# Kernel tuning notes

Measured on AMD Instinct MI355X. Metric: run time of the kernel, lower is better.

Reference implementation:

```python
import jax, jax.numpy as jnp
import numpy as np

T, B, H, L = 512, 64, 100, 10  # seq_len, batch, hidden, num_layers


def setup_inputs() -> dict:
    key = jax.random.key(0)
    ks = jax.random.split(key, 8)
    s = 0.1  # ~ PyTorch uniform(-1/sqrt(H), 1/sqrt(H)) scale
    return {
        "x": jax.random.normal(ks[0], (T, B, H), jnp.float32),
        "W_ih0": jax.random.normal(ks[1], (2, H, H), jnp.float32) * s,
        "W_ih": jax.random.normal(ks[2], (L - 1, 2, H, 2 * H), jnp.float32) * s,
        "W_hh": jax.random.normal(ks[3], (L, 2, H, H), jnp.float32) * s,
        "b_ih": jax.random.normal(ks[4], (L, 2, H), jnp.float32) * s,
        "b_hh": jax.random.normal(ks[5], (L, 2, H), jnp.float32) * s,
        "W_out": jax.random.normal(ks[6], (1, 2 * H), jnp.float32) * s,
        "b_out": jax.random.normal(ks[7], (1,), jnp.float32) * s,
    }


def _rnn_dir(x, Wih, Whh, b, reverse):
    # Precompute input projection for all timesteps as one big GEMM.
    # z: [T, B, H]; b already holds b_ih + b_hh.
    z = jnp.einsum('tbi,hi->tbh', x, Wih) + b
    h0 = jnp.zeros((x.shape[1], Whh.shape[0]), x.dtype)

    def step(h, zt):
        h = jnp.tanh(zt + h @ Whh.T)
        return h, h

    # reverse=True scans backward in time but emits outputs in original order,
    # exactly matching the backward direction of a bidirectional RNN.
    _, ys = jax.lax.scan(step, h0, z, reverse=reverse)
    return ys  # [T, B, H]


def reference(x, W_ih0, W_ih, W_hh, b_ih, b_hh, W_out, b_out):
    h = x
    for l in range(L):
        Wih_l = W_ih0 if l == 0 else W_ih[l - 1]
        fwd = _rnn_dir(h, Wih_l[0], W_hh[l, 0], b_ih[l, 0] + b_hh[l, 0], False)
        bwd = _rnn_dir(h, Wih_l[1], W_hh[l, 1], b_ih[l, 1] + b_hh[l, 1], True)
        h = jnp.concatenate([fwd, bwd], axis=-1)  # [T, B, 2H]
    y = jax.nn.sigmoid(jnp.einsum('tbh,oh->tbo', h, W_out) + b_out)  # [T, B, 1]
    return y.reshape(-1)  # [T*B]
```

## Files before the change

### kernel.cpp

```cpp
#include <hip/hip_runtime.h>
#include <math.h>


#define T_LEN 512
#define BATCH 64
#define HID   100
#define M_TOT (T_LEN * BATCH)

__global__ __launch_bounds__(256) void ingemm_kernel(
    const float* __restrict__ In, const float* __restrict__ W,
    const float* __restrict__ bih, const float* __restrict__ bhh,
    float* __restrict__ z, int K)
{
    __shared__ float As[16][68];
    __shared__ float Bs[16][68];
    const int tid = threadIdx.x;
    const int m0 = blockIdx.x * 64;
    const int n0 = blockIdx.y * 64;
    const int tx = tid & 15, ty = tid >> 4;
    const int lm = tid >> 2;
    const int lk = (tid & 3) << 2;

    float acc[4][4];
    #pragma unroll
    for (int i = 0; i < 4; ++i)
        #pragma unroll
        for (int j = 0; j < 4; ++j) acc[i][j] = 0.f;

    for (int k0 = 0; k0 < K; k0 += 16) {
        float4 av = make_float4(0.f,0.f,0.f,0.f);
        float4 bv = make_float4(0.f,0.f,0.f,0.f);
        if (k0 + lk < K)
            av = *(const float4*)(In + (size_t)(m0 + lm) * K + k0 + lk);
        const int nrow = n0 + lm;
        if (nrow < 200 && k0 + lk < K)
            bv = *(const float4*)(W + (size_t)nrow * K + k0 + lk);
        As[lk+0][lm]=av.x; As[lk+1][lm]=av.y; As[lk+2][lm]=av.z; As[lk+3][lm]=av.w;
        Bs[lk+0][lm]=bv.x; Bs[lk+1][lm]=bv.y; Bs[lk+2][lm]=bv.z; Bs[lk+3][lm]=bv.w;
        __syncthreads();
        #pragma unroll
        for (int kk = 0; kk < 16; ++kk) {
            float4 a4 = *(const float4*)&As[kk][ty << 2];
            float4 b4 = *(const float4*)&Bs[kk][tx << 2];
            float a[4] = {a4.x, a4.y, a4.z, a4.w};
            float b[4] = {b4.x, b4.y, b4.z, b4.w};
            #pragma unroll
            for (int i = 0; i < 4; ++i)
                #pragma unroll
                for (int j = 0; j < 4; ++j)
                    acc[i][j] += a[i] * b[j];
        }
        __syncthreads();
    }
    #pragma unroll
    for (int i = 0; i < 4; ++i) {
        const int m = m0 + (ty << 2) + i;
        #pragma unroll
        for (int j = 0; j < 4; ++j) {
            const int n = n0 + (tx << 2) + j;
            if (n < 200) {
                const int dir = (n >= 100) ? 1 : 0;
                const int h = n - dir * 100;
                z[(size_t)dir * M_TOT * HID + (size_t)m * HID + h] =
                    acc[i][j] + bih[n] + bhh[n];
            }
        }
    }
}

__device__ __forceinline__ float dpp_qxor1(float x) {
    int i = __float_as_int(x);
    i = __builtin_amdgcn_update_dpp(0, i, 0xB1, 0xF, 0xF, false);
    return __int_as_float(i);
}
__device__ __forceinline__ float dpp_qxor2(float x) {
    int i = __float_as_int(x);
    i = __builtin_amdgcn_update_dpp(0, i, 0x4E, 0xF, 0xF, false);
    return __int_as_float(i);
}

__global__ __launch_bounds__(256) void scan_kernel(
    const float* __restrict__ z,
    const float* __restrict__ Whh,
    float* __restrict__ out)
{
    const int dir = blockIdx.x >> 6;
    const int b   = blockIdx.x & 63;
    const int tid = threadIdx.x;
    const int w   = tid >> 6;
    const int lane= tid & 63;
    const int ks  = lane & 3;
    const int jslot = lane >> 2;
    const int jj  = w + 4 * jslot;
    const bool active = (jj < 50);
    const int jjc = active ? jj : 49;
    const int kb  = 28 * ks;
    const int jout = 2 * jjc + (ks & 1);
    const bool writer = active && (ks < 2);

    __shared__ float h_lds[2][128];
    for (int i = tid; i < 256; i += 256) (&h_lds[0][0])[i] = 0.f;

    float w2[2][28];
    #pragma unroll
    for (int r = 0; r < 2; ++r) {
        const float* wr = Whh + ((size_t)dir * HID + 2 * jjc + r) * HID + kb;
        #pragma unroll
        for (int q = 0; q < 7; ++q) {
            float4 v = make_float4(0.f, 0.f, 0.f, 0.f);
            if (kb + 4 * q + 3 < HID)
                v = *(const float4*)(wr + 4 * q);
            w2[r][4*q+0] = v.x; w2[r][4*q+1] = v.y;
            w2[r][4*q+2] = v.z; w2[r][4*q+3] = v.w;
        }
    }
    __syncthreads();

    const ptrdiff_t zstride = BATCH * HID;
    const ptrdiff_t ostride = BATCH * 200;
    const int t0 = dir ? (T_LEN - 1) : 0;
    const ptrdiff_t zstep = dir ? -zstride : zstride;
    const ptrdiff_t ostep = dir ? -ostride : ostride;
    const ptrdiff_t zstep2 = 2 * zstep, zstep3 = 3 * zstep, zstep4 = 4 * zstep;

    const float* zp = z + (size_t)dir * M_TOT * HID + (size_t)b * HID + jout
                        + (ptrdiff_t)t0 * zstride;
    float*       op = out + (size_t)b * 200 + dir * HID + jout
                        + (ptrdiff_t)t0 * ostride;

    float zr0 = zp[0];
    float zr1 = zp[zstep];
    float zr2 = zp[zstep2];
    float zr3 = zp[zstep3];
    const float* zpf = zp + zstep4;

#define RNN_STEP(ZREG, DO_PF, PFOFF, RD, WRB)                           \
  do {                                                                  \
    const float zin = ZREG;                                             \
    if (DO_PF) ZREG = *(zpf + (PFOFF));   \
    const float4* hp = (const float4*)((RD) + kb);                      \
    float a0 = 0.f, a1 = 0.f;                                           \
    _Pragma("unroll")                                                   \
    for (int q = 0; q < 7; ++q) {                                       \
      float4 hv = hp[q];                                                \
      a0 += w2[0][4*q+0] * hv.x; a0 += w2[0][4*q+1] * hv.y;             \
      a0 += w2[0][4*q+2] * hv.z; a0 += w2[0][4*q+3] * hv.w;             \
      a1 += w2[1][4*q+0] * hv.x; a1 += w2[1][4*q+1] * hv.y;             \
      a1 += w2[1][4*q+2] * hv.z; a1 += w2[1][4*q+3] * hv.w;             \
    }                                                                   \
            \
    float keep = (ks & 1) ? a1 : a0;                                    \
    float send = (ks & 1) ? a0 : a1;                                    \
    float s = keep + dpp_qxor1(send);                                   \
          \
    float tot = s + dpp_qxor2(s);                                       \
    float xin = zin + tot;                                              \
    float ax = fabsf(xin);                                              \
    float e = __expf(2.f * ax);                                         \
    float r = 1.f - 2.f / (e + 1.f);                                    \
    float val = copysignf(r, xin);                                      \
    if (writer) {                                                       \
      (WRB)[jout] = val;                                                \
      *op = val;                                                        \
    }                                                                   \
    op += ostep;                                                        \
    asm volatile("s_waitcnt lgkmcnt(0)" ::: "memory");                  \
    __builtin_amdgcn_sched_barrier(0);                                  \
    __builtin_amdgcn_s_barrier();                                       \
    __builtin_amdgcn_sched_barrier(0);                                  \
  } while (0)

    float* const h0 = &h_lds[0][0];
    float* const h1 = &h_lds[1][0];

    for (int g = 0; g < (T_LEN / 4) - 1; ++g) {
        RNN_STEP(zr0, 1, 0,      h0, h1);
        RNN_STEP(zr1, 1, zstep,  h1, h0);
        RNN_STEP(zr2, 1, zstep2, h0, h1);
        RNN_STEP(zr3, 1, zstep3, h1, h0);
        zpf += zstep4;
    }
    RNN_STEP(zr0, 0, 0, h0, h1);
    RNN_STEP(zr1, 0, 0, h1, h0);
    RNN_STEP(zr2, 0, 0, h0, h1);
    RNN_STEP(zr3, 0, 0, h1, h0);

#undef RNN_STEP
}

__global__ __launch_bounds__(256) void outproj_kernel(
    const float* __restrict__ h, const float* __restrict__ Wout,
    const float* __restrict__ bout, float* __restrict__ y)
{
    const int gid = blockIdx.x * 256 + threadIdx.x;
    const int wid = gid >> 6;
    const int lane = threadIdx.x & 63;
    if (wid >= M_TOT) return;
    const float* row = h + (size_t)wid * 200;
    float acc = 0.f;
    for (int k = lane; k < 200; k += 64) acc += row[k] * Wout[k];
    #pragma unroll
    for (int off = 32; off > 0; off >>= 1) acc += __shfl_xor(acc, off);
    if (lane == 0) y[wid] = 1.f / (1.f + __expf(-(acc + bout[0])));
}

extern "C" void kernel_launch(void* const* d_in, const int* in_sizes, int n_in,
                              void* d_out, int out_size, void* d_ws, size_t ws_size,
                              hipStream_t stream)
{
    const float* x     = (const float*)d_in[0];
    const float* W_ih0 = (const float*)d_in[1];
    const float* W_ih  = (const float*)d_in[2];
    const float* W_hh  = (const float*)d_in[3];
    const float* b_ih  = (const float*)d_in[4];
    const float* b_hh  = (const float*)d_in[5];
    const float* W_out = (const float*)d_in[6];
    const float* b_out = (const float*)d_in[7];
    float* y = (float*)d_out;

    float* z    = (float*)d_ws;
    float* buf0 = z + (size_t)2 * M_TOT * HID;
    float* buf1 = buf0 + (size_t)M_TOT * 200;

    for (int l = 0; l < 10; ++l) {
        const float* In = (l == 0) ? x : ((l & 1) ? buf0 : buf1);
        float* Out      = (l & 1) ? buf1 : buf0;
        const int K     = (l == 0) ? 100 : 200;
        const float* W  = (l == 0) ? W_ih0 : (W_ih + (size_t)(l - 1) * 2 * 100 * 200);
        ingemm_kernel<<<dim3(M_TOT / 64, 4), 256, 0, stream>>>(
            In, W, b_ih + l * 200, b_hh + l * 200, z, K);
        scan_kernel<<<128, 256, 0, stream>>>(
            z, W_hh + (size_t)l * 2 * HID * HID, Out);
    }
    outproj_kernel<<<M_TOT / 4, 256, 0, stream>>>(buf1, W_out, b_out, y);
}
```

Measured before the change: 2.201 ms.

## Retile input-projection GEMM to 128x100 per-direction blocks with 8x5 microtiles

Rewrites the input-projection GEMM so each block covers 128 rows and one full direction (100 outputs), using 320 threads with an 8x5 register microtile and a K step of 20. This removes the wasted padded columns (the old 4x64 N-tiling covered 256 columns for 200 outputs) and the per-element bounds checks, and raises arithmetic intensity per shared-memory load. The bias sum is hoisted into registers. The cost is higher register pressure and odd-stride shared-memory access patterns that may cause bank conflicts. The GEMM is likely a minor share of total time next to the sequential scan.

```diff
diff --git a/kernel.cpp b/kernel.cpp
--- a/kernel.cpp
+++ b/kernel.cpp
@@ -7,64 +7,86 @@
 #define HID   100
 #define M_TOT (T_LEN * BATCH)
 
-__global__ __launch_bounds__(256) void ingemm_kernel(
+__global__ __launch_bounds__(320) void ingemm_kernel(
     const float* __restrict__ In, const float* __restrict__ W,
     const float* __restrict__ bih, const float* __restrict__ bhh,
     float* __restrict__ z, int K)
 {
-    __shared__ float As[16][68];
-    __shared__ float Bs[16][68];
+    __shared__ float As[20][132];
+    __shared__ float Bs[20][200];
+
     const int tid = threadIdx.x;
-    const int m0 = blockIdx.x * 64;
-    const int n0 = blockIdx.y * 64;
-    const int tx = tid & 15, ty = tid >> 4;
-    const int lm = tid >> 2;
-    const int lk = (tid & 3) << 2;
-
-    float acc[4][4];
-    #pragma unroll
-    for (int i = 0; i < 4; ++i)
-        #pragma unroll
-        for (int j = 0; j < 4; ++j) acc[i][j] = 0.f;
-
-    for (int k0 = 0; k0 < K; k0 += 16) {
-        float4 av = make_float4(0.f,0.f,0.f,0.f);
-        float4 bv = make_float4(0.f,0.f,0.f,0.f);
-        if (k0 + lk < K)
-            av = *(const float4*)(In + (size_t)(m0 + lm) * K + k0 + lk);
-        const int nrow = n0 + lm;
-        if (nrow < 200 && k0 + lk < K)
-            bv = *(const float4*)(W + (size_t)nrow * K + k0 + lk);
-        As[lk+0][lm]=av.x; As[lk+1][lm]=av.y; As[lk+2][lm]=av.z; As[lk+3][lm]=av.w;
-        Bs[lk+0][lm]=bv.x; Bs[lk+1][lm]=bv.y; Bs[lk+2][lm]=bv.z; Bs[lk+3][lm]=bv.w;
+    const int tx  = tid % 20;
+    const int ty  = tid / 20;
+    const int m0  = blockIdx.x * 128;
+    const int dir = blockIdx.y;
+
+    const float* Wd = W + (size_t)dir * HID * K;
+
+    float bsum[5];
+    #pragma unroll
+    for (int j = 0; j < 5; ++j) {
+        const int n = dir * HID + tx * 5 + j;
+        bsum[j] = bih[n] + bhh[n];
+    }
+
+    float acc[8][5];
+    #pragma unroll
+    for (int i = 0; i < 8; ++i)
+        #pragma unroll
+        for (int j = 0; j < 5; ++j) acc[i][j] = 0.f;
+
+    for (int k0 = 0; k0 < K; k0 += 20) {
+        #pragma unroll
+        for (int rep = 0; rep < 2; ++rep) {
+            const int idx = tid + rep * 320;
+            const int row = idx / 5;
+            const int c   = idx % 5;
+            float4 v = *(const float4*)(In + (size_t)(m0 + row) * K + k0 + 4 * c);
+            As[4*c+0][row] = v.x; As[4*c+1][row] = v.y;
+            As[4*c+2][row] = v.z; As[4*c+3][row] = v.w;
+        }
+        #pragma unroll
+        for (int rep = 0; rep < 2; ++rep) {
+            const int idx = tid + rep * 320;
+            if (idx < 500) {
+                const int n = idx / 5;
+                const int c = idx % 5;
+                float4 v = *(const float4*)(Wd + (size_t)n * K + k0 + 4 * c);
+                const int col = (n / 5) * 10 + (n % 5);
+                Bs[4*c+0][col] = v.x; Bs[4*c+1][col] = v.y;
+                Bs[4*c+2][col] = v.z; Bs[4*c+3][col] = v.w;
+            }
+        }
         __syncthreads();
-        #pragma unroll
-        for (int kk = 0; kk < 16; ++kk) {
-            float4 a4 = *(const float4*)&As[kk][ty << 2];
-            float4 b4 = *(const float4*)&Bs[kk][tx << 2];
-            float a[4] = {a4.x, a4.y, a4.z, a4.w};
-            float b[4] = {b4.x, b4.y, b4.z, b4.w};
+
+        #pragma unroll
+        for (int kk = 0; kk < 20; ++kk) {
+            float4 alo = *(const float4*)&As[kk][ty * 4];
+            float4 ahi = *(const float4*)&As[kk][64 + ty * 4];
+            float a[8] = {alo.x, alo.y, alo.z, alo.w,
+                          ahi.x, ahi.y, ahi.z, ahi.w};
+            float2 b01 = *(const float2*)&Bs[kk][tx * 10];
+            float2 b23 = *(const float2*)&Bs[kk][tx * 10 + 2];
+            float  b4  = Bs[kk][tx * 10 + 4];
+            float b[5] = {b01.x, b01.y, b23.x, b23.y, b4};
             #pragma unroll
-            for (int i = 0; i < 4; ++i)
+            for (int i = 0; i < 8; ++i)
                 #pragma unroll
-                for (int j = 0; j < 4; ++j)
+                for (int j = 0; j < 5; ++j)
                     acc[i][j] += a[i] * b[j];
         }
         __syncthreads();
     }
-    #pragma unroll
-    for (int i = 0; i < 4; ++i) {
-        const int m = m0 + (ty << 2) + i;
-        #pragma unroll
-        for (int j = 0; j < 4; ++j) {
-            const int n = n0 + (tx << 2) + j;
-            if (n < 200) {
-                const int dir = (n >= 100) ? 1 : 0;
-                const int h = n - dir * 100;
-                z[(size_t)dir * M_TOT * HID + (size_t)m * HID + h] =
-                    acc[i][j] + bih[n] + bhh[n];
-            }
-        }
+
+    float* zd = z + (size_t)dir * M_TOT * HID;
+    #pragma unroll
+    for (int i = 0; i < 8; ++i) {
+        const int m = m0 + ((i < 4) ? (ty * 4 + i) : (64 + ty * 4 + (i - 4)));
+        float* zr = zd + (size_t)m * HID + tx * 5;
+        #pragma unroll
+        for (int j = 0; j < 5; ++j)
+            zr[j] = acc[i][j] + bsum[j];
     }
 }
 
@@ -227,7 +249,7 @@
         float* Out      = (l & 1) ? buf1 : buf0;
         const int K     = (l == 0) ? 100 : 200;
         const float* W  = (l == 0) ? W_ih0 : (W_ih + (size_t)(l - 1) * 2 * 100 * 200);
-        ingemm_kernel<<<dim3(M_TOT / 64, 4), 256, 0, stream>>>(
+        ingemm_kernel<<<dim3(M_TOT / 128, 2), 320, 0, stream>>>(
             In, W, b_ih + l * 200, b_hh + l * 200, z, K);
         scan_kernel<<<128, 256, 0, stream>>>(
             z, W_hh + (size_t)l * 2 * HID * HID, Out);
```

After: 2.355 ms. +7.0%, slower.

## Repartition recurrent matvec to 8 K-chunk lanes per 4 output rows

Applied to the files above, without the earlier changes.

The scan kernel's per-step h·Whh^T work is remapped so each group of 8 lanes owns 4 output rows and splits K into 8 overlapping 16-wide chunks. Chunk overlap is handled by zeroing the first 4 weights. Partial sums are combined with a row_half_mirror DPP followed by quad-xor DPP selects. This shortens each lane's dependent FMA chain and its LDS reads per step, which should cut latency on the serial recurrence. In exchange it adds more total FMAs, extra DPP and select instructions, and more weight registers.

```diff
diff --git a/kernel.cpp b/kernel.cpp
--- a/kernel.cpp
+++ b/kernel.cpp
@@ -78,6 +78,11 @@
     i = __builtin_amdgcn_update_dpp(0, i, 0x4E, 0xF, 0xF, false);
     return __int_as_float(i);
 }
+__device__ __forceinline__ float dpp_hmir(float x) {
+    int i = __float_as_int(x);
+    i = __builtin_amdgcn_update_dpp(0, i, 0x141, 0xF, 0xF, false);
+    return __int_as_float(i);
+}
 
 __global__ __launch_bounds__(256) void scan_kernel(
     const float* __restrict__ z,
@@ -89,29 +94,31 @@
     const int tid = threadIdx.x;
     const int w   = tid >> 6;
     const int lane= tid & 63;
-    const int ks  = lane & 3;
-    const int jslot = lane >> 2;
-    const int jj  = w + 4 * jslot;
-    const bool active = (jj < 50);
-    const int jjc = active ? jj : 49;
-    const int kb  = 28 * ks;
-    const int jout = 2 * jjc + (ks & 1);
-    const bool writer = active && (ks < 2);
-
-    __shared__ float h_lds[2][128];
-    for (int i = tid; i < 256; i += 256) (&h_lds[0][0])[i] = 0.f;
-
-    float w2[2][28];
-    #pragma unroll
-    for (int r = 0; r < 2; ++r) {
-        const float* wr = Whh + ((size_t)dir * HID + 2 * jjc + r) * HID + kb;
-        #pragma unroll
-        for (int q = 0; q < 7; ++q) {
-            float4 v = make_float4(0.f, 0.f, 0.f, 0.f);
-            if (kb + 4 * q + 3 < HID)
-                v = *(const float4*)(wr + 4 * q);
-            w2[r][4*q+0] = v.x; w2[r][4*q+1] = v.y;
-            w2[r][4*q+2] = v.z; w2[r][4*q+3] = v.w;
+    const int q   = lane & 3;
+    const int b2  = (lane >> 2) & 1;
+    const int ks  = q | (b2 << 2);
+    const int slot= (lane >> 3) + 8 * w;
+    const bool active = (slot < 25);
+    const int slotc = active ? slot : 24;
+    const int jout = 4 * slotc + q;
+    const bool writer = active && (b2 == 0);
+    const int kb = 12 * ks;
+
+    __shared__ float h_lds[2][112];
+    for (int i = tid; i < 224; i += 256) (&h_lds[0][0])[i] = 0.f;
+
+    float w4[4][16];
+    #pragma unroll
+    for (int r = 0; r < 4; ++r) {
+        const float* wr = Whh + ((size_t)dir * HID + 4 * slotc + r) * HID + kb;
+        #pragma unroll
+        for (int i = 0; i < 4; ++i) {
+            float4 v = *(const float4*)(wr + 4 * i);
+            w4[r][4*i+0] = v.x; w4[r][4*i+1] = v.y;
+            w4[r][4*i+2] = v.z; w4[r][4*i+3] = v.w;
+        }
+        if (ks > 0) {
+            w4[r][0] = 0.f; w4[r][1] = 0.f; w4[r][2] = 0.f; w4[r][3] = 0.f;
         }
     }
     __syncthreads();
@@ -139,21 +146,35 @@
     const float zin = ZREG;                                             \
     if (DO_PF) ZREG = *(zpf + (PFOFF));   \
     const float4* hp = (const float4*)((RD) + kb);                      \
-    float a0 = 0.f, a1 = 0.f;                                           \
+    float a0 = 0.f, a1 = 0.f, a2 = 0.f, a3 = 0.f;                       \
     _Pragma("unroll")                                                   \
-    for (int q = 0; q < 7; ++q) {                                       \
-      float4 hv = hp[q];                                                \
-      a0 += w2[0][4*q+0] * hv.x; a0 += w2[0][4*q+1] * hv.y;             \
-      a0 += w2[0][4*q+2] * hv.z; a0 += w2[0][4*q+3] * hv.w;             \
-      a1 += w2[1][4*q+0] * hv.x; a1 += w2[1][4*q+1] * hv.y;             \
-      a1 += w2[1][4*q+2] * hv.z; a1 += w2[1][4*q+3] * hv.w;             \
+    for (int i = 0; i < 4; ++i) {                                       \
+      float4 hv = hp[i];                                                \
+      a0 += w4[0][4*i+0] * hv.x; a0 += w4[0][4*i+1] * hv.y;             \
+      a0 += w4[0][4*i+2] * hv.z; a0 += w4[0][4*i+3] * hv.w;             \
+      a1 += w4[1][4*i+0] * hv.x; a1 += w4[1][4*i+1] * hv.y;             \
+      a1 += w4[1][4*i+2] * hv.z; a1 += w4[1][4*i+3] * hv.w;             \
+      a2 += w4[2][4*i+0] * hv.x; a2 += w4[2][4*i+1] * hv.y;             \
+      a2 += w4[2][4*i+2] * hv.z; a2 += w4[2][4*i+3] * hv.w;             \
+      a3 += w4[3][4*i+0] * hv.x; a3 += w4[3][4*i+1] * hv.y;             \
+      a3 += w4[3][4*i+2] * hv.z; a3 += w4[3][4*i+3] * hv.w;             \
     }                                                                   \
-            \
-    float keep = (ks & 1) ? a1 : a0;                                    \
-    float send = (ks & 1) ? a0 : a1;                                    \
-    float s = keep + dpp_qxor1(send);                                   \
-          \
-    float tot = s + dpp_qxor2(s);                                       \
+           \
+    float t0_ = a0 + dpp_hmir(a0);                                      \
+    float t1_ = a1 + dpp_hmir(a1);                                      \
+    float t2_ = a2 + dpp_hmir(a2);                                      \
+    float t3_ = a3 + dpp_hmir(a3);                                      \
+                                     \
+    float k01 = (q & 1) ? t1_ : t0_;                                    \
+    float s01s = (q & 1) ? t0_ : t1_;                                   \
+    float s01 = k01 + dpp_qxor1(s01s);                                  \
+    float k23 = (q & 1) ? t3_ : t2_;                                    \
+    float s23s = (q & 1) ? t2_ : t3_;                                   \
+    float s23 = k23 + dpp_qxor1(s23s);                                  \
+        \
+    float kf = (q & 2) ? s23 : s01;                                     \
+    float sf = (q & 2) ? s01 : s23;                                     \
+    float tot = kf + dpp_qxor2(sf);                                     \
     float xin = zin + tot;                                              \
     float ax = fabsf(xin);                                              \
     float e = __expf(2.f * ax);                                         \
```

Measured after the change: 2.204 ms. No clear change (+0.1%).
